# Kernel tuning notes

Hardware: AMD Instinct MI355X
Metric: run time of the kernel (lower is better)

## Reference

```python
import jax, jax.numpy as jnp
import numpy as np

B, L, D, MAXL = 4, 2048, 1024, 4096

def setup_inputs() -> dict:
    key = jax.random.key(0)
    ks = jax.random.split(key, 7)
    x = jax.random.normal(ks[0], (B, L, D), dtype=jnp.float32)
    mask = jnp.ones((B, 1, L), dtype=jnp.int32)
    # kv_proj: Linear(D,D) -> ReLU -> Linear(D, 2D)
    s1 = 1.0 / np.sqrt(D)
    W1 = jax.random.uniform(ks[1], (D, D), minval=-s1, maxval=s1, dtype=jnp.float32)
    b1 = jax.random.uniform(ks[2], (D,), minval=-s1, maxval=s1, dtype=jnp.float32)
    W2 = jax.random.uniform(ks[3], (D, 2 * D), minval=-s1, maxval=s1, dtype=jnp.float32)
    b2 = jax.random.uniform(ks[4], (2 * D,), minval=-s1, maxval=s1, dtype=jnp.float32)
    D_to_L = jax.random.normal(ks[5], (D, MAXL), dtype=jnp.float32) * 0.01
    return {"x": x, "mask": mask, "W1": W1, "b1": b1, "W2": W2, "b2": b2, "D_to_L": D_to_L}

def reference(x, mask, W1, b1, W2, b2, D_to_L):
    Lcur = x.shape[1]
    h = jax.nn.relu(x @ W1 + b1)          # [B,L,D]
    kv = h @ W2 + b2                       # [B,L,2D]
    k, value = jnp.split(kv, 2, axis=-1)   # [B,L,D] each
    scores = jnp.einsum('bld,dk->blk', k, D_to_L[:, :Lcur])  # [B,L,L]
    scores = jnp.where(mask == 0, -jnp.inf, scores)
    attention = jax.nn.softmax(scores, axis=-1)
    output = attention @ value             # [B,L,D]
    return output, attention
```

## Files before the change

kernel.cpp:

```cpp
#include <hip/hip_runtime.h>
#include <cstdint>
#include <cstddef>

__device__ __forceinline__ float bf2f(uint16_t u) {
    union { uint32_t i; float f; } w; w.i = ((uint32_t)u) << 16; return w.f;
}
__device__ __forceinline__ uint16_t f2bf(float f) {
    union { float f; uint32_t i; } w; w.f = f;
    uint32_t x = w.i;
    uint32_t r = (x + 0x7FFFu + ((x >> 16) & 1u)) >> 16;
    return (uint16_t)r;
}

typedef __bf16 bf16x8 __attribute__((ext_vector_type(8)));
typedef float  f32x4  __attribute__((ext_vector_type(4)));

__device__ __forceinline__ void load_lds16(const void* gptr, void* lptr) {
    __builtin_amdgcn_global_load_lds(
        (__attribute__((address_space(1))) void*)gptr,
        (__attribute__((address_space(3))) void*)lptr,
        16, 0, 0);
}

template<int OUTFP32, int RELU, int SPLIT>
__global__ __launch_bounds__(256, 3)
void gemm_bt(const uint16_t* __restrict__ A, const uint16_t* __restrict__ BT,
             const float* __restrict__ bias, void* __restrict__ Cv,
             int K, int lda, int ldb, int ldc,
             long long sA, long long sB, long long sC,
             void* __restrict__ C2v, int ldc2, int ncut)
{
    __shared__ uint16_t As[128 * 32];
    __shared__ uint16_t Bs[128 * 32];

    const int nx = (int)gridDim.x, ny = (int)gridDim.y, nz = (int)gridDim.z;
    const int g   = (int)blockIdx.x + nx * ((int)blockIdx.y + ny * (int)blockIdx.z);
    const int xcd = g & 7;
    const int ii  = g >> 3;
    const int xz  = 8 / nz;
    const int bz  = xcd / xz;
    const int sub = xcd % xz;
    const int ypc = ny / xz;
    const int by  = sub * ypc + ii % ypc;
    const int bx  = ii / ypc;

    const int t    = threadIdx.x;
    const int lane = t & 63;
    const int w    = t >> 6;
    const int quad = lane >> 4;
    const int l15  = lane & 15;
    const int wr   = w >> 1;
    const int wc   = w & 1;
    const int gm0  = by * 128;
    const int gn0  = bx * 128;

    A  += (long long)bz * sA;
    BT += (long long)bz * sB;

    f32x4 acc[4][4] = {};

    const int ch_r = lane >> 2;
    const int ch_c = (lane & 3) * 8;

    for (int k0 = 0; k0 < K; k0 += 32) {
        __syncthreads();
        {
            int row = w * 16 + ch_r;
            load_lds16(BT + (size_t)(gn0 + row) * ldb + k0 + ch_c, (void*)(Bs + w * 512));
            load_lds16(BT + (size_t)(gn0 + row + 64) * ldb + k0 + ch_c, (void*)(Bs + (w + 4) * 512));
            load_lds16(A + (size_t)(gm0 + row) * lda + k0 + ch_c, (void*)(As + w * 512));
            load_lds16(A + (size_t)(gm0 + row + 64) * lda + k0 + ch_c, (void*)(As + (w + 4) * 512));
        }
        __syncthreads();

        bf16x8 af[4], bfr[4];
#pragma unroll
        for (int i = 0; i < 4; i++) {
            af[i]  = *(const bf16x8*)(As + (wr * 64 + i * 16 + l15) * 32 + quad * 8);
            bfr[i] = *(const bf16x8*)(Bs + (wc * 64 + i * 16 + l15) * 32 + quad * 8);
        }
#pragma unroll
        for (int mi = 0; mi < 4; mi++)
#pragma unroll
            for (int ni = 0; ni < 4; ni++)
                acc[mi][ni] = __builtin_amdgcn_mfma_f32_16x16x32_bf16(af[mi], bfr[ni], acc[mi][ni], 0, 0, 0);
    }

    const bool to2 = SPLIT && (gn0 >= ncut);
#pragma unroll
    for (int ni = 0; ni < 4; ni++) {
        const int gcol = gn0 + wc * 64 + ni * 16 + l15;
        const float bv = (!to2 && bias) ? bias[gcol] : 0.0f;
#pragma unroll
        for (int mi = 0; mi < 4; mi++) {
#pragma unroll
            for (int r = 0; r < 4; r++) {
                const int grow = gm0 + wr * 64 + mi * 16 + quad * 4 + r;
                float v = acc[mi][ni][r] + bv;
                if (RELU) v = fmaxf(v, 0.0f);
                if (to2) {
                    uint16_t* C2 = (uint16_t*)C2v;
                    C2[(size_t)grow * ldc2 + (gcol - ncut)] = f2bf(v);
                } else if (OUTFP32) {
                    float* C = (float*)Cv + (long long)bz * sC;
                    C[(size_t)grow * ldc + gcol] = v;
                } else {
                    uint16_t* C = (uint16_t*)Cv + (long long)bz * sC;
                    C[(size_t)grow * ldc + gcol] = f2bf(v);
                }
            }
        }
    }
}

__global__ __launch_bounds__(256)
void cast_f32_bf16(const float* __restrict__ src, uint16_t* __restrict__ dst)
{
    const size_t i = ((size_t)blockIdx.x * 256 + threadIdx.x) * 8;
    float4 f0 = *(const float4*)(src + i);
    float4 f1 = *(const float4*)(src + i + 4);
    uint16_t u[8];
    u[0] = f2bf(f0.x); u[1] = f2bf(f0.y); u[2] = f2bf(f0.z); u[3] = f2bf(f0.w);
    u[4] = f2bf(f1.x); u[5] = f2bf(f1.y); u[6] = f2bf(f1.z); u[7] = f2bf(f1.w);
    *(uint4*)(dst + i) = *(const uint4*)u;
}

__global__ __launch_bounds__(256)
void cast2d_f32_bf16(const float* __restrict__ src, uint16_t* __restrict__ dst,
                     int src_ld, int C)
{
    const size_t i = ((size_t)blockIdx.x * 256 + threadIdx.x) * 8;
    const int r = (int)(i / C), c = (int)(i % C);
    const float* sp = src + (size_t)r * src_ld + c;
    float4 f0 = *(const float4*)sp;
    float4 f1 = *(const float4*)(sp + 4);
    uint16_t u[8];
    u[0] = f2bf(f0.x); u[1] = f2bf(f0.y); u[2] = f2bf(f0.z); u[3] = f2bf(f0.w);
    u[4] = f2bf(f1.x); u[5] = f2bf(f1.y); u[6] = f2bf(f1.z); u[7] = f2bf(f1.w);
    *(uint4*)(dst + i) = *(const uint4*)u;
}

__global__ __launch_bounds__(256)
void transpose_f32_to_bf16(const float* __restrict__ src, uint16_t* __restrict__ dst,
                           int src_ld, int dst_ld)
{
    __shared__ uint16_t tile[64 * 65];
    const int k0 = blockIdx.y * 64, n0 = blockIdx.x * 64;
    const int t = threadIdx.x;
#pragma unroll
    for (int i = 0; i < 16; i++) {
        int idx = i * 256 + t;
        int r = idx >> 6, c = idx & 63;
        tile[c * 65 + r] = f2bf(src[(size_t)(k0 + r) * src_ld + n0 + c]);
    }
    __syncthreads();
#pragma unroll
    for (int i = 0; i < 16; i++) {
        int idx = i * 256 + t;
        int n = idx >> 6, k = idx & 63;
        dst[(size_t)(n0 + n) * dst_ld + k0 + k] = tile[n * 65 + k];
    }
}

__global__ __launch_bounds__(256)
void transpose_bf16(const uint16_t* __restrict__ src, uint16_t* __restrict__ dst,
                    int src_ld, int dst_ld, long long sS, long long sD)
{
    __shared__ uint16_t tile[64 * 65];
    src += (long long)blockIdx.z * sS;
    dst += (long long)blockIdx.z * sD;
    const int k0 = blockIdx.y * 64, n0 = blockIdx.x * 64;
    const int t = threadIdx.x;
#pragma unroll
    for (int i = 0; i < 16; i++) {
        int idx = i * 256 + t;
        int r = idx >> 6, c = idx & 63;
        tile[c * 65 + r] = src[(size_t)(k0 + r) * src_ld + n0 + c];
    }
    __syncthreads();
#pragma unroll
    for (int i = 0; i < 16; i++) {
        int idx = i * 256 + t;
        int n = idx >> 6, k = idx & 63;
        dst[(size_t)(n0 + n) * dst_ld + k0 + k] = tile[n * 65 + k];
    }
}

__global__ __launch_bounds__(256)
void colbias(const float* __restrict__ b2, const float* __restrict__ D2L,
             float* __restrict__ out)
{
    const int l = blockIdx.x * 256 + threadIdx.x;
    float acc = 0.f;
#pragma unroll 8
    for (int d = 0; d < 1024; d++)
        acc = fmaf(b2[d], D2L[(size_t)d * 4096 + l], acc);
    out[l] = acc;
}

__global__ __launch_bounds__(256)
void softmax_rows(const uint16_t* __restrict__ Sin_, float* __restrict__ Aout,
                  uint16_t* __restrict__ Abf, const float* __restrict__ bs,
                  const int* __restrict__ mask, int L)
{
    const int row = blockIdx.x;
    const int b = row >> 11;
    const uint16_t* sp = Sin_ + (size_t)row * L;
    float* op = Aout + (size_t)row * L;
    uint16_t* bp = Abf + (size_t)row * L;
    const int* mrow = mask + (size_t)b * L;
    const int t = threadIdx.x;
    const int c0 = t * 8;

    uint16_t su[8];
    *(uint4*)su = *(const uint4*)(sp + c0);
    float v[8];
    bool mk[8];
    float lmax = -1e30f;
#pragma unroll
    for (int j = 0; j < 8; j++) {
        mk[j] = (mrow[c0 + j] != 0);
        v[j] = bf2f(su[j]) + bs[c0 + j];
        if (mk[j]) lmax = fmaxf(lmax, v[j]);
    }
#pragma unroll
    for (int off = 32; off > 0; off >>= 1)
        lmax = fmaxf(lmax, __shfl_xor(lmax, off, 64));

    __shared__ float redm[4];
    __shared__ float reds[4];
    const int w = t >> 6, lane = t & 63;
    if (lane == 0) redm[w] = lmax;
    __syncthreads();
    lmax = fmaxf(fmaxf(redm[0], redm[1]), fmaxf(redm[2], redm[3]));

    float e[8];
    float lsum = 0.f;
#pragma unroll
    for (int j = 0; j < 8; j++) {
        e[j] = mk[j] ? __expf(v[j] - lmax) : 0.0f;
        lsum += e[j];
    }
#pragma unroll
    for (int off = 32; off > 0; off >>= 1)
        lsum += __shfl_xor(lsum, off, 64);
    if (lane == 0) reds[w] = lsum;
    __syncthreads();
    lsum = reds[0] + reds[1] + reds[2] + reds[3];

    const float inv = 1.0f / lsum;
    uint16_t ub[8];
#pragma unroll
    for (int j = 0; j < 8; j++) {
        v[j] = e[j] * inv;
        ub[j] = f2bf(v[j]);
    }
    *(float4*)(op + c0)     = *(const float4*)(v + 0);
    *(float4*)(op + c0 + 4) = *(const float4*)(v + 4);
    *(uint4*)(bp + c0)      = *(const uint4*)ub;
}

extern "C" void kernel_launch(void* const* d_in, const int* in_sizes, int n_in,
                              void* d_out, int out_size, void* d_ws, size_t ws_size,
                              hipStream_t stream)
{
    const float* x    = (const float*)d_in[0];
    const int*   mask = (const int*)d_in[1];
    const float* W1   = (const float*)d_in[2];
    const float* b1   = (const float*)d_in[3];
    const float* W2   = (const float*)d_in[4];
    const float* b2   = (const float*)d_in[5];
    const float* D2L  = (const float*)d_in[6];

    const int Lr = 2048, D = 1024, M = 4 * Lr;
    float* outp = (float*)d_out;
    float* attn = outp + (size_t)M * D;

    uint16_t* W1T    = (uint16_t*)d_ws;
    uint16_t* BTcat  = W1T   + 1024 * 1024;
    uint16_t* D2LT   = BTcat + 3072 * 1024;
    uint16_t* W2kbf  = D2LT  + 2048 * 1024;
    float*    bias_s = (float*)(W2kbf + 1024 * 1024);
    uint16_t* xbf    = (uint16_t*)(bias_s + 2048);
    uint16_t* hbuf   = xbf  + (size_t)M * D;
    uint16_t* Vbuf   = hbuf + (size_t)M * D;
    uint16_t* Sbf    = Vbuf + (size_t)M * D;
    uint16_t* vT     = Sbf  + (size_t)M * 2048;

    dim3 blk(256);

    cast_f32_bf16<<<dim3(4096), blk, 0, stream>>>(x, xbf);
    transpose_f32_to_bf16<<<dim3(16, 16), blk, 0, stream>>>(W1, W1T, 1024, 1024);
    transpose_f32_to_bf16<<<dim3(16, 16), blk, 0, stream>>>(W2 + 1024, BTcat, 2048, 1024);
    transpose_f32_to_bf16<<<dim3(32, 16), blk, 0, stream>>>(D2L, D2LT, 4096, 1024);
    cast2d_f32_bf16<<<dim3(512), blk, 0, stream>>>(W2, W2kbf, 2048, 1024);
    colbias<<<dim3(8), blk, 0, stream>>>(b2, D2L, bias_s);

    gemm_bt<0, 0, 0><<<dim3(8, 16, 1), blk, 0, stream>>>(D2LT, W2kbf, nullptr,
        BTcat + 1024 * 1024, 1024, 1024, 1024, 1024, 0, 0, 0, nullptr, 0, 0);

    gemm_bt<0, 1, 0><<<dim3(8, 64, 1), blk, 0, stream>>>(xbf, W1T, b1, hbuf,
        1024, 1024, 1024, 1024, 0, 0, 0, nullptr, 0, 0);

    gemm_bt<0, 0, 1><<<dim3(24, 64, 1), blk, 0, stream>>>(hbuf, BTcat, b2 + 1024, Vbuf,
        1024, 1024, 1024, 1024, 0, 0, 0, Sbf, 2048, 1024);

    transpose_bf16<<<dim3(16, 32, 4), blk, 0, stream>>>(Vbuf, vT,
        1024, 2048, (long long)2048 * 1024, (long long)1024 * 2048);

    softmax_rows<<<dim3(8192), blk, 0, stream>>>(Sbf, attn, Sbf, bias_s, mask, Lr);

    gemm_bt<1, 0, 0><<<dim3(8, 16, 4), blk, 0, stream>>>(Sbf, vT, nullptr, outp,
        2048, 2048, 2048, 1024,
        (long long)2048 * 2048, (long long)1024 * 2048, (long long)2048 * 1024,
        nullptr, 0, 0);
}
```

Before: 399.8 us.

## Deepen GEMM K-step to 64, split fused V/score GEMM, reuse workspace buffers

The GEMM main loop now stages two 32-wide K slices per iteration into doubled LDS buffers, which halves the number of barrier pairs per tile. The fused SPLIT GEMM that wrote both V and the score matrix is replaced by two separate GEMM launches, which removes the per-tile output branching. Workspace buffers are aliased (V reuses the x-bf16 buffer, vT reuses h) to shrink the memory footprint. The larger LDS footprint (32KB per block) may reduce occupancy below the requested 3 blocks per CU. Reading h twice across two launches adds global traffic.

Result: faster. 385.3 us (-3.6%).

```diff
diff --git a/kernel.cpp b/kernel.cpp
--- a/kernel.cpp
+++ b/kernel.cpp
@@ -22,16 +22,15 @@
         16, 0, 0);
 }
 
-template<int OUTFP32, int RELU, int SPLIT>
+template<int OUTFP32, int RELU>
 __global__ __launch_bounds__(256, 3)
 void gemm_bt(const uint16_t* __restrict__ A, const uint16_t* __restrict__ BT,
              const float* __restrict__ bias, void* __restrict__ Cv,
              int K, int lda, int ldb, int ldc,
-             long long sA, long long sB, long long sC,
-             void* __restrict__ C2v, int ldc2, int ncut)
-{
-    __shared__ uint16_t As[128 * 32];
-    __shared__ uint16_t Bs[128 * 32];
+             long long sA, long long sB, long long sC)
+{
+    __shared__ uint16_t As[2][128 * 32];
+    __shared__ uint16_t Bs[2][128 * 32];
 
     const int nx = (int)gridDim.x, ny = (int)gridDim.y, nz = (int)gridDim.z;
     const int g   = (int)blockIdx.x + nx * ((int)blockIdx.y + ny * (int)blockIdx.z);
@@ -62,35 +61,45 @@
     const int ch_r = lane >> 2;
     const int ch_c = (lane & 3) * 8;
 
-    for (int k0 = 0; k0 < K; k0 += 32) {
+    for (int k0 = 0; k0 < K; k0 += 64) {
         __syncthreads();
         {
-            int row = w * 16 + ch_r;
-            load_lds16(BT + (size_t)(gn0 + row) * ldb + k0 + ch_c, (void*)(Bs + w * 512));
-            load_lds16(BT + (size_t)(gn0 + row + 64) * ldb + k0 + ch_c, (void*)(Bs + (w + 4) * 512));
-            load_lds16(A + (size_t)(gm0 + row) * lda + k0 + ch_c, (void*)(As + w * 512));
-            load_lds16(A + (size_t)(gm0 + row + 64) * lda + k0 + ch_c, (void*)(As + (w + 4) * 512));
+            const int row = w * 16 + ch_r;
+            const size_t bo0 = (size_t)(gn0 + row) * ldb + k0 + ch_c;
+            const size_t bo1 = (size_t)(gn0 + row + 64) * ldb + k0 + ch_c;
+            const size_t ao0 = (size_t)(gm0 + row) * lda + k0 + ch_c;
+            const size_t ao1 = (size_t)(gm0 + row + 64) * lda + k0 + ch_c;
+            load_lds16(BT + bo0,      (void*)(Bs[0] + w * 512));
+            load_lds16(BT + bo1,      (void*)(Bs[0] + (w + 4) * 512));
+            load_lds16(BT + bo0 + 32, (void*)(Bs[1] + w * 512));
+            load_lds16(BT + bo1 + 32, (void*)(Bs[1] + (w + 4) * 512));
+            load_lds16(A + ao0,       (void*)(As[0] + w * 512));
+            load_lds16(A + ao1,       (void*)(As[0] + (w + 4) * 512));
+            load_lds16(A + ao0 + 32,  (void*)(As[1] + w * 512));
+            load_lds16(A + ao1 + 32,  (void*)(As[1] + (w + 4) * 512));
         }
         __syncthreads();
 
-        bf16x8 af[4], bfr[4];
-#pragma unroll
-        for (int i = 0; i < 4; i++) {
-            af[i]  = *(const bf16x8*)(As + (wr * 64 + i * 16 + l15) * 32 + quad * 8);
-            bfr[i] = *(const bf16x8*)(Bs + (wc * 64 + i * 16 + l15) * 32 + quad * 8);
+#pragma unroll
+        for (int s = 0; s < 2; s++) {
+            bf16x8 af[4], bfr[4];
+#pragma unroll
+            for (int i = 0; i < 4; i++) {
+                af[i]  = *(const bf16x8*)(As[s] + (wr * 64 + i * 16 + l15) * 32 + quad * 8);
+                bfr[i] = *(const bf16x8*)(Bs[s] + (wc * 64 + i * 16 + l15) * 32 + quad * 8);
+            }
+#pragma unroll
+            for (int mi = 0; mi < 4; mi++)
+#pragma unroll
+                for (int ni = 0; ni < 4; ni++)
+                    acc[mi][ni] = __builtin_amdgcn_mfma_f32_16x16x32_bf16(af[mi], bfr[ni], acc[mi][ni], 0, 0, 0);
         }
-#pragma unroll
-        for (int mi = 0; mi < 4; mi++)
-#pragma unroll
-            for (int ni = 0; ni < 4; ni++)
-                acc[mi][ni] = __builtin_amdgcn_mfma_f32_16x16x32_bf16(af[mi], bfr[ni], acc[mi][ni], 0, 0, 0);
-    }
-
-    const bool to2 = SPLIT && (gn0 >= ncut);
+    }
+
 #pragma unroll
     for (int ni = 0; ni < 4; ni++) {
         const int gcol = gn0 + wc * 64 + ni * 16 + l15;
-        const float bv = (!to2 && bias) ? bias[gcol] : 0.0f;
+        const float bv = bias ? bias[gcol] : 0.0f;
 #pragma unroll
         for (int mi = 0; mi < 4; mi++) {
 #pragma unroll
@@ -98,10 +107,7 @@
                 const int grow = gm0 + wr * 64 + mi * 16 + quad * 4 + r;
                 float v = acc[mi][ni][r] + bv;
                 if (RELU) v = fmaxf(v, 0.0f);
-                if (to2) {
-                    uint16_t* C2 = (uint16_t*)C2v;
-                    C2[(size_t)grow * ldc2 + (gcol - ncut)] = f2bf(v);
-                } else if (OUTFP32) {
+                if (OUTFP32) {
                     float* C = (float*)Cv + (long long)bz * sC;
                     C[(size_t)grow * ldc + gcol] = v;
                 } else {
@@ -277,41 +283,44 @@
     float* attn = outp + (size_t)M * D;
 
     uint16_t* W1T    = (uint16_t*)d_ws;
-    uint16_t* BTcat  = W1T   + 1024 * 1024;
-    uint16_t* D2LT   = BTcat + 3072 * 1024;
+    uint16_t* W2vT   = W1T   + 1024 * 1024;
+    uint16_t* W2DT   = W2vT  + 1024 * 1024;
+    uint16_t* D2LT   = W2DT  + 2048 * 1024;
     uint16_t* W2kbf  = D2LT  + 2048 * 1024;
     float*    bias_s = (float*)(W2kbf + 1024 * 1024);
     uint16_t* xbf    = (uint16_t*)(bias_s + 2048);
     uint16_t* hbuf   = xbf  + (size_t)M * D;
-    uint16_t* Vbuf   = hbuf + (size_t)M * D;
-    uint16_t* Sbf    = Vbuf + (size_t)M * D;
-    uint16_t* vT     = Sbf  + (size_t)M * 2048;
+    uint16_t* Sbf    = hbuf + (size_t)M * D;
+    uint16_t* Vbuf   = xbf;
+    uint16_t* vT     = hbuf;
 
     dim3 blk(256);
 
     cast_f32_bf16<<<dim3(4096), blk, 0, stream>>>(x, xbf);
     transpose_f32_to_bf16<<<dim3(16, 16), blk, 0, stream>>>(W1, W1T, 1024, 1024);
-    transpose_f32_to_bf16<<<dim3(16, 16), blk, 0, stream>>>(W2 + 1024, BTcat, 2048, 1024);
+    transpose_f32_to_bf16<<<dim3(16, 16), blk, 0, stream>>>(W2 + 1024, W2vT, 2048, 1024);
     transpose_f32_to_bf16<<<dim3(32, 16), blk, 0, stream>>>(D2L, D2LT, 4096, 1024);
     cast2d_f32_bf16<<<dim3(512), blk, 0, stream>>>(W2, W2kbf, 2048, 1024);
     colbias<<<dim3(8), blk, 0, stream>>>(b2, D2L, bias_s);
 
-    gemm_bt<0, 0, 0><<<dim3(8, 16, 1), blk, 0, stream>>>(D2LT, W2kbf, nullptr,
-        BTcat + 1024 * 1024, 1024, 1024, 1024, 1024, 0, 0, 0, nullptr, 0, 0);
-
-    gemm_bt<0, 1, 0><<<dim3(8, 64, 1), blk, 0, stream>>>(xbf, W1T, b1, hbuf,
-        1024, 1024, 1024, 1024, 0, 0, 0, nullptr, 0, 0);
-
-    gemm_bt<0, 0, 1><<<dim3(24, 64, 1), blk, 0, stream>>>(hbuf, BTcat, b2 + 1024, Vbuf,
-        1024, 1024, 1024, 1024, 0, 0, 0, Sbf, 2048, 1024);
+    gemm_bt<0, 0><<<dim3(8, 16, 1), blk, 0, stream>>>(D2LT, W2kbf, nullptr, W2DT,
+        1024, 1024, 1024, 1024, 0, 0, 0);
+
+    gemm_bt<0, 1><<<dim3(8, 64, 1), blk, 0, stream>>>(xbf, W1T, b1, hbuf,
+        1024, 1024, 1024, 1024, 0, 0, 0);
+
+    gemm_bt<0, 0><<<dim3(8, 64, 1), blk, 0, stream>>>(hbuf, W2vT, b2 + 1024, Vbuf,
+        1024, 1024, 1024, 1024, 0, 0, 0);
+
+    gemm_bt<0, 0><<<dim3(16, 64, 1), blk, 0, stream>>>(hbuf, W2DT, nullptr, Sbf,
+        1024, 1024, 1024, 2048, 0, 0, 0);
 
     transpose_bf16<<<dim3(16, 32, 4), blk, 0, stream>>>(Vbuf, vT,
         1024, 2048, (long long)2048 * 1024, (long long)1024 * 2048);
 
     softmax_rows<<<dim3(8192), blk, 0, stream>>>(Sbf, attn, Sbf, bias_s, mask, Lr);
 
-    gemm_bt<1, 0, 0><<<dim3(8, 16, 4), blk, 0, stream>>>(Sbf, vT, nullptr, outp,
+    gemm_bt<1, 0><<<dim3(8, 16, 4), blk, 0, stream>>>(Sbf, vT, nullptr, outp,
         2048, 2048, 2048, 1024,
-        (long long)2048 * 2048, (long long)1024 * 2048, (long long)2048 * 1024,
-        nullptr, 0, 0);
-}
+        (long long)2048 * 2048, (long long)1024 * 2048, (long long)2048 * 1024);
+}
```
